# Optimization experiments

Measured on AMD Instinct MI355X. Metric: run time of the kernel, lower is better.

The kernel has to match this reference:

```python
import jax, jax.numpy as jnp
import numpy as np

B, T, D, H, W = 128, 1024, 32, 64, 128
C = D + 1            # control_size = data_size + 1
O = H * C            # cvf MLP output size


def _linear_params(k, out_f, in_f):
    lim = 1.0 / np.sqrt(in_f)
    kw, kb = jax.random.split(k)
    Wm = jax.random.uniform(kw, (out_f, in_f), minval=-lim, maxval=lim, dtype=jnp.float32)
    b = jax.random.uniform(kb, (out_f,), minval=-lim, maxval=lim, dtype=jnp.float32)
    return Wm, b


def setup_inputs() -> dict:
    key = jax.random.key(0)
    ks = jax.random.split(key, 8)
    # initial MLP: (D+1) -> W -> W -> H, relu hidden
    iW0, ib0 = _linear_params(ks[0], W, D + 1)
    iW1, ib1 = _linear_params(ks[1], W, W)
    iW2, ib2 = _linear_params(ks[2], H, W)
    # cvf MLP: (H+1) -> W -> W -> H*C, lipswish hidden, tanh final
    vW0, vb0 = _linear_params(ks[3], W, H + 1)
    vW1, vb1 = _linear_params(ks[4], W, W)
    vW2, vb2 = _linear_params(ks[5], O, W)
    # readout: H -> 1
    rW, rb = _linear_params(ks[6], 1, H)
    ts = jnp.arange(T, dtype=jnp.float32)
    ys = jax.random.normal(ks[7], (B, T, D), dtype=jnp.float32)
    return dict(ts=ts, ys=ys,
                iW0=iW0, ib0=ib0, iW1=iW1, ib1=ib1, iW2=iW2, ib2=ib2,
                vW0=vW0, vb0=vb0, vW1=vb1 * 0 + vW1, vb1=vb1, vW2=vW2, vb2=vb2,
                rW=rW, rb=rb)


def _lipswish(x):
    return 0.909 * jax.nn.silu(x)


def reference(ts, ys, iW0, ib0, iW1, ib1, iW2, ib2,
              vW0, vb0, vW1, vb1, vW2, vb2, rW, rb):
    b, t_len, d = ys.shape
    h = iW2.shape[0]
    c = d + 1

    def initial_mlp(x):  # [B, D+1] -> [B, H]
        z = jax.nn.relu(x @ iW0.T + ib0)
        z = jax.nn.relu(z @ iW1.T + ib1)
        return z @ iW2.T + ib2

    def vf(t, y):  # scalar t, y [B,H] -> [B,H,C]
        inp = jnp.concatenate([jnp.full((y.shape[0], 1), t, y.dtype), y], axis=1)
        z = _lipswish(inp @ vW0.T + vb0)
        z = _lipswish(z @ vW1.T + vb1)
        out = jnp.tanh(z @ vW2.T + vb2)
        return out.reshape(y.shape[0], h, c)

    # control path values x(t_i) = [t_i, y_i]; no NaNs so interpolation fixups are no-ops
    xs = jnp.concatenate([jnp.broadcast_to(ts[None, :, None], (b, t_len, 1)), ys], axis=2)  # [B,T,C]
    y0 = initial_mlp(xs[:, 0])
    vf0 = vf(ts[0], y0)

    # constant step dt=1 aligned with grid -> control increments are consecutive diffs
    dxs = jnp.swapaxes(xs[:, 1:] - xs[:, :-1], 0, 1)  # [T-1,B,C]
    t1s = ts[1:]

    def step(carry, inp):
        y, yhat, v = carry
        t1, dx = inp
        # ReversibleHeun: yhat1 = 2*y - yhat + f(t0,yhat0)·dx ; y1 = y + 0.5*(f0+f1)·dx
        yhat1 = 2.0 * y - yhat + jnp.einsum('bhc,bc->bh', v, dx)
        v1 = vf(t1, yhat1)
        y1 = y + 0.5 * jnp.einsum('bhc,bc->bh', v + v1, dx)
        return (y1, yhat1, v1), None

    (yT, _, _), _ = jax.lax.scan(step, (y0, y0, vf0), (t1s, dxs))
    return yT @ rW.T + rb  # [B,1]
```

## Files before the change

kernel.cpp:

```cpp
#include <hip/hip_runtime.h>
#include <math.h>

constexpr int kB  = 128;
constexpr int kT  = 1024;
constexpr int kD  = 32;
constexpr int kH  = 64;
constexpr int kW  = 128;
constexpr int kC  = kD + 1;
constexpr int kO  = kH * kC;
constexpr int kIN = kH + 1;
constexpr int BLOCK = 1024;

constexpr int WS_W2  = 0;
constexpr int WS_W1  = 135168;
constexpr int WS_W0  = 143360;
constexpr int WS_SC2 = 147584;
constexpr int WS_SC1 = 149696;
constexpr int WS_SC0 = 149824;
constexpr int WS_TOT = 149952;

__device__ __forceinline__ float fast_sigmoid(float x) { return 1.0f / (1.0f + __expf(-x)); }
__device__ __forceinline__ float lipswish_f(float x)   { return 0.909f * x * fast_sigmoid(x); }
__device__ __forceinline__ float fast_tanh(float x) {
    float ax = fabsf(x);
    float e  = __expf(2.0f * ax);
    float r  = 1.0f - 2.0f / (e + 1.0f);
    return copysignf(r, x);
}
__device__ __forceinline__ float dot4(float4 a, float4 b) {
    return a.x * b.x + a.y * b.y + a.z * b.z + a.w * b.w;
}
__device__ __forceinline__ float fma2i(unsigned u, float z0, float z1, float acc) {
    int lo = (int)(short)(u & 0xffffu);
    int hi = ((int)u) >> 16;
    acc += (float)lo * z0 + (float)hi * z1;
    return acc;
}
__device__ __forceinline__ float fma8i(uint4 u, float4 zl, float4 zh, float acc) {
    acc = fma2i(u.x, zl.x, zl.y, acc);
    acc = fma2i(u.y, zl.z, zl.w, acc);
    acc = fma2i(u.z, zh.x, zh.y, acc);
    acc = fma2i(u.w, zh.z, zh.w, acc);
    return acc;
}
__device__ __forceinline__ int q15(float w, float inv) {
    float q = rintf(w * inv);
    q = fmaxf(-32767.0f, fminf(32767.0f, q));
    return (int)q;
}
__device__ __forceinline__ unsigned pack16(int a, int b) {
    return ((unsigned)a & 0xffffu) | ((unsigned)b << 16);
}

__global__ __launch_bounds__(64)
void prep_kernel(const float* __restrict__ vW0, const float* __restrict__ vW1,
                 const float* __restrict__ vW2, unsigned* __restrict__ ws)
{
    const int row  = blockIdx.x;
    const int lane = threadIdx.x;
    float* scf = (float*)ws;

    if (row < kO) {
        const float* src = vW2 + (size_t)row * kW;
        float m = fmaxf(fabsf(src[lane]), fabsf(src[lane + 64]));
        #pragma unroll
        for (int s = 1; s < 64; s <<= 1) m = fmaxf(m, __shfl_xor(m, s));
        float inv = (m > 0.0f) ? 32767.0f / m : 0.0f;
        if (lane == 0) scf[WS_SC2 + row] = (m > 0.0f) ? m / 32767.0f : 0.0f;
        int w = lane;
        unsigned pk = pack16(q15(src[2 * w], inv), q15(src[2 * w + 1], inv));
        int R = row >> 6, r = row & 63, q = w >> 2, e = w & 3;
        ws[WS_W2 + (((R * 16 + q) * 64 + r) << 2) + e] = pk;
    } else if (row < kO + kW) {
        int r = row - kO;
        const float* src = vW1 + (size_t)r * kW;
        float m = fmaxf(fabsf(src[lane]), fabsf(src[lane + 64]));
        #pragma unroll
        for (int s = 1; s < 64; s <<= 1) m = fmaxf(m, __shfl_xor(m, s));
        float inv = (m > 0.0f) ? 32767.0f / m : 0.0f;
        if (lane == 0) scf[WS_SC1 + r] = (m > 0.0f) ? m / 32767.0f : 0.0f;
        int w = lane;
        ws[WS_W1 + r * 64 + w] = pack16(q15(src[2 * w], inv), q15(src[2 * w + 1], inv));
    } else {
        int r = row - kO - kW;
        const float* src = vW0 + (size_t)r * kIN;
        float m = fabsf(src[lane]);
        if (lane == 0) m = fmaxf(m, fabsf(src[64]));
        #pragma unroll
        for (int s = 1; s < 64; s <<= 1) m = fmaxf(m, __shfl_xor(m, s));
        float inv = (m > 0.0f) ? 32767.0f / m : 0.0f;
        if (lane == 0) scf[WS_SC0 + r] = (m > 0.0f) ? m / 32767.0f : 0.0f;
        if (lane < 33) {
            int c0 = 2 * lane, c1 = 2 * lane + 1;
            int qa = q15(src[c0], inv);
            int qb = (c1 < kIN) ? q15(src[c1], inv) : 0;
            ws[WS_W0 + r * 33 + lane] = pack16(qa, qb);
        }
    }
}

template <int QI>
__global__ __launch_bounds__(BLOCK)
void cde_kernel(
    const float* __restrict__ ts,  const float* __restrict__ ys,
    const float* __restrict__ iW0, const float* __restrict__ ib0,
    const float* __restrict__ iW1, const float* __restrict__ ib1,
    const float* __restrict__ iW2, const float* __restrict__ ib2,
    const float* __restrict__ vW0, const float* __restrict__ vb0,
    const float* __restrict__ vW1, const float* __restrict__ vb1,
    const float* __restrict__ vW2, const float* __restrict__ vb2,
    const float* __restrict__ rW,  const float* __restrict__ rb,
    const unsigned* __restrict__ wsb,
    float* __restrict__ out)
{
    const int b  = blockIdx.x;
    const int t  = threadIdx.x;
    const int r8 = t >> 3;
    const int g  = t & 7;
    const int wv = t >> 6;
    const int ln = t & 63;

    __shared__ __align__(16) float s_v[kO];
    __shared__ __align__(16) float s_z1[kW], s_z2[kW];
    __shared__ __align__(16) float s_inp[kIN + 1];
    __shared__ float s_y[kH], s_yhat[kH], s_e[kH];
    __shared__ float s_dx[kC];

    const float*    ysb   = ys + (size_t)b * kT * kD;
    const uint4*    wsW2q = (const uint4*)(wsb + WS_W2);
    const unsigned* wsW1  = wsb + WS_W1;
    const unsigned* wsW0  = wsb + WS_W0;
    const float*    scf   = (const float*)wsb;

    const float bA  = vb2[t];
    const float bB  = vb2[t + 1024];
    const float bTl = (t < 512) ? vb2[2048 + r8] : 0.0f;
    const float b0r = vb0[r8];
    const float b1r = vb1[r8];
    const float sA  = QI ? scf[WS_SC2 + t] : 0.0f;
    const float sB  = QI ? scf[WS_SC2 + t + 1024] : 0.0f;
    const float sTl = (QI && t < 512) ? scf[WS_SC2 + 2048 + r8] : 0.0f;
    const float s0r = QI ? scf[WS_SC0 + r8] : 0.0f;
    const float s1r = QI ? scf[WS_SC1 + r8] : 0.0f;

    float x_reg = 0.0f, x_next = 0.0f;
    if (t < kC) {
        x_reg  = (t == 0) ? ts[0] : ysb[t - 1];
        x_next = (t == 0) ? ts[1] : ysb[kD + (t - 1)];
        s_dx[t] = x_reg;
    }
    if (t == 0) s_inp[kIN] = 0.0f;
    __syncthreads();

    if (t < kW) {
        const float* wrow = iW0 + t * kC;
        float acc = ib0[t];
        #pragma unroll
        for (int c = 0; c < kC; c++) acc += wrow[c] * s_dx[c];
        s_z1[t] = fmaxf(acc, 0.0f);
    }
    __syncthreads();
    if (t < kW) {
        const float4* wr = (const float4*)(iW1 + t * kW);
        const float4* z4 = (const float4*)s_z1;
        float acc = ib1[t];
        #pragma unroll 8
        for (int q = 0; q < kW / 4; q++) acc += dot4(wr[q], z4[q]);
        s_z2[t] = fmaxf(acc, 0.0f);
    }
    __syncthreads();
    if (t < kH) {
        const float4* wr = (const float4*)(iW2 + t * kW);
        const float4* z4 = (const float4*)s_z2;
        float acc = ib2[t];
        #pragma unroll 8
        for (int q = 0; q < kW / 4; q++) acc += dot4(wr[q], z4[q]);
        s_y[t] = acc; s_yhat[t] = acc;
        s_inp[1 + t] = acc;
    }
    if (t == 0) s_inp[0] = x_reg;
    __syncthreads();

    for (int i = 0; i < kT; i++) {
        {
            float acc = 0.0f;
            if (QI) {
                const unsigned* rowp = wsW0 + r8 * 33;
                #pragma unroll
                for (int m = 0; m < 5; m++) {
                    int p = g + 8 * m;
                    if (p < 33) acc = fma2i(rowp[p], s_inp[2 * p], s_inp[2 * p + 1], acc);
                }
            } else {
                const float* rowp = vW0 + r8 * kIN;
                #pragma unroll
                for (int m = 0; m < 5; m++) {
                    int p = g + 8 * m;
                    if (p < 33) {
                        float w0 = rowp[2 * p];
                        float w1 = (2 * p + 1 < kIN) ? rowp[2 * p + 1] : 0.0f;
                        acc += w0 * s_inp[2 * p] + w1 * s_inp[2 * p + 1];
                    }
                }
            }
            acc += __shfl_xor(acc, 1);
            acc += __shfl_xor(acc, 2);
            acc += __shfl_xor(acc, 4);
            if (g == 0) s_z1[r8] = lipswish_f(b0r + (QI ? s0r * acc : acc));
        }
        __syncthreads();
        {
            float acc = 0.0f;
            #pragma unroll
            for (int m = 0; m < 2; m++) {
                int ch = g + 8 * m;
                int c0 = 8 * ch;
                const float4* z4 = (const float4*)(s_z1 + c0);
                float4 za = z4[0], zb = z4[1];
                if (QI) {
                    uint4 u = *(const uint4*)(wsW1 + r8 * 64 + 4 * ch);
                    acc = fma8i(u, za, zb, acc);
                } else {
                    const float* wr = vW1 + r8 * kW + c0;
                    acc += dot4(*(const float4*)wr, za) + dot4(*(const float4*)(wr + 4), zb);
                }
            }
            acc += __shfl_xor(acc, 1);
            acc += __shfl_xor(acc, 2);
            acc += __shfl_xor(acc, 4);
            if (g == 0) s_z2[r8] = lipswish_f(b1r + (QI ? s1r * acc : acc));
        }
        __syncthreads();
        {
            float acc0 = 0.0f, acc1 = 0.0f;
            if (QI) {
                const uint4* pA = wsW2q + (size_t)(wv * 16) * 64 + ln;
                const uint4* pB = wsW2q + (size_t)((wv + 16) * 16) * 64 + ln;
                #pragma unroll 2
                for (int m = 0; m < 8; m++) {
                    const float4* z4 = (const float4*)(s_z2 + 16 * m);
                    float4 z0 = z4[0], z1 = z4[1], z2 = z4[2], z3 = z4[3];
                    uint4 a0 = pA[(2 * m) * 64],     a1 = pA[(2 * m + 1) * 64];
                    uint4 c0 = pB[(2 * m) * 64],     c1 = pB[(2 * m + 1) * 64];
                    acc0 = fma8i(a0, z0, z1, acc0);
                    acc0 = fma8i(a1, z2, z3, acc0);
                    acc1 = fma8i(c0, z0, z1, acc1);
                    acc1 = fma8i(c1, z2, z3, acc1);
                }
                s_v[t]        = fast_tanh(bA + sA * acc0);
                s_v[t + 1024] = fast_tanh(bB + sB * acc1);
            } else {
                #pragma unroll 2
                for (int m = 0; m < 8; m++) {
                    const float4* z4 = (const float4*)(s_z2 + 16 * m);
                    float4 z0 = z4[0], z1 = z4[1], z2 = z4[2], z3 = z4[3];
                    const float4* rA = (const float4*)(vW2 + (size_t)t * kW + 16 * m);
                    const float4* rB = (const float4*)(vW2 + (size_t)(t + 1024) * kW + 16 * m);
                    acc0 += dot4(rA[0], z0) + dot4(rA[1], z1) + dot4(rA[2], z2) + dot4(rA[3], z3);
                    acc1 += dot4(rB[0], z0) + dot4(rB[1], z1) + dot4(rB[2], z2) + dot4(rB[3], z3);
                }
                s_v[t]        = fast_tanh(bA + acc0);
                s_v[t + 1024] = fast_tanh(bB + acc1);
            }
        }
        if (t < 512) {
            int c0 = 16 * g;
            const float4* z4 = (const float4*)(s_z2 + c0);
            float4 z0 = z4[0], z1 = z4[1], z2 = z4[2], z3 = z4[3];
            float acc = 0.0f;
            if (QI) {
                uint4 u0 = wsW2q[(size_t)(32 * 16 + 2 * g) * 64 + r8];
                uint4 u1 = wsW2q[(size_t)(32 * 16 + 2 * g + 1) * 64 + r8];
                acc = fma8i(u0, z0, z1, acc);
                acc = fma8i(u1, z2, z3, acc);
            } else {
                const float4* wr = (const float4*)(vW2 + (size_t)(2048 + r8) * kW + c0);
                acc += dot4(wr[0], z0) + dot4(wr[1], z1) + dot4(wr[2], z2) + dot4(wr[3], z3);
            }
            acc += __shfl_xor(acc, 1);
            acc += __shfl_xor(acc, 2);
            acc += __shfl_xor(acc, 4);
            if (g == 0) s_v[2048 + r8] = fast_tanh(bTl + (QI ? sTl * acc : acc));
        }
        __syncthreads();

        if (i > 0 && t < kH) {
            const float* vr = s_v + t * kC;
            float acc = 0.0f;
            #pragma unroll
            for (int c = 0; c < kC; c++) acc += vr[c] * s_dx[c];
            s_y[t] += 0.5f * (s_e[t] + acc);
        }
        __syncthreads();

        if (i < kT - 1) {
            if (t < kC) {
                float xi = x_next;
                s_dx[t] = xi - x_reg;
                x_reg = xi;
                if (i + 2 < kT)
                    x_next = (t == 0) ? ts[i + 2] : ysb[(size_t)(i + 2) * kD + (t - 1)];
            }
            __syncthreads();
            if (t < kH) {
                const float* vr = s_v + t * kC;
                float e = 0.0f;
                #pragma unroll
                for (int c = 0; c < kC; c++) e += vr[c] * s_dx[c];
                s_e[t] = e;
                float yh = 2.0f * s_y[t] - s_yhat[t] + e;
                s_yhat[t] = yh;
                s_inp[1 + t] = yh;
            }
            if (t == 0) s_inp[0] = x_reg;
            __syncthreads();
        }
    }

    __syncthreads();
    if (t == 0) {
        float acc = rb[0];
        #pragma unroll
        for (int h = 0; h < kH; h++) acc += s_y[h] * rW[h];
        out[b] = acc;
    }
}

extern "C" void kernel_launch(void* const* d_in, const int* in_sizes, int n_in,
                              void* d_out, int out_size, void* d_ws, size_t ws_size,
                              hipStream_t stream)
{
    const float* ts  = (const float*)d_in[0];
    const float* ys  = (const float*)d_in[1];
    const float* iW0 = (const float*)d_in[2];
    const float* ib0 = (const float*)d_in[3];
    const float* iW1 = (const float*)d_in[4];
    const float* ib1 = (const float*)d_in[5];
    const float* iW2 = (const float*)d_in[6];
    const float* ib2 = (const float*)d_in[7];
    const float* vW0 = (const float*)d_in[8];
    const float* vb0 = (const float*)d_in[9];
    const float* vW1 = (const float*)d_in[10];
    const float* vb1 = (const float*)d_in[11];
    const float* vW2 = (const float*)d_in[12];
    const float* vb2 = (const float*)d_in[13];
    const float* rW  = (const float*)d_in[14];
    const float* rb  = (const float*)d_in[15];
    float* out = (float*)d_out;
    unsigned* ws = (unsigned*)d_ws;

    if (ws_size >= (size_t)WS_TOT * 4) {
        hipLaunchKernelGGL(prep_kernel, dim3(kO + kW + kW), dim3(64), 0, stream,
                           vW0, vW1, vW2, ws);
        hipLaunchKernelGGL((cde_kernel<1>), dim3(kB), dim3(BLOCK), 0, stream,
                           ts, ys, iW0, ib0, iW1, ib1, iW2, ib2,
                           vW0, vb0, vW1, vb1, vW2, vb2, rW, rb, ws, out);
    } else {
        hipLaunchKernelGGL((cde_kernel<0>), dim3(kB), dim3(BLOCK), 0, stream,
                           ts, ys, iW0, ib0, iW1, ib1, iW2, ib2,
                           vW0, vb0, vW1, vb1, vW2, vb2, rW, rb, ws, out);
    }
}
```

Before: 6.456 ms.

## Split each batch's vector field across two cooperating blocks with flag sync

Adds a kernel that launches two blocks per batch element. Each block computes half of the cvf output rows (1056 of 2112) and updates half of the hidden state. The halves of yhat are exchanged every step through global memory, using agent-scope release/acquire flags and a double-buffered exchange buffer. This aims to halve the per-step final-layer work per block and use all 256 CUs instead of 128, at the cost of a cross-block spin-wait each timestep. Correctness depends on both blocks of a pair being co-resident.

```diff
diff --git a/kernel.cpp b/kernel.cpp
--- a/kernel.cpp
+++ b/kernel.cpp
@@ -18,6 +18,9 @@
 constexpr int WS_SC1 = 149696;
 constexpr int WS_SC0 = 149824;
 constexpr int WS_TOT = 149952;
+constexpr int WS_XB   = 149952;
+constexpr int WS_FLAG = 166336;
+constexpr int WS_TOT2 = 166592;
 
 __device__ __forceinline__ float fast_sigmoid(float x) { return 1.0f / (1.0f + __expf(-x)); }
 __device__ __forceinline__ float lipswish_f(float x)   { return 0.909f * x * fast_sigmoid(x); }
@@ -61,6 +64,7 @@
     float* scf = (float*)ws;
 
     if (row < kO) {
+        if (row < 4) ws[WS_FLAG + row * 64 + lane] = 0;
         const float* src = vW2 + (size_t)row * kW;
         float m = fmaxf(fabsf(src[lane]), fabsf(src[lane + 64]));
         #pragma unroll
@@ -99,9 +103,240 @@
     }
 }
 
+__global__ __launch_bounds__(BLOCK)
+void cde_split(
+    const float* __restrict__ ts,  const float* __restrict__ ys,
+    const float* __restrict__ iW0, const float* __restrict__ ib0,
+    const float* __restrict__ iW1, const float* __restrict__ ib1,
+    const float* __restrict__ iW2, const float* __restrict__ ib2,
+    const float* __restrict__ vW0, const float* __restrict__ vb0,
+    const float* __restrict__ vW1, const float* __restrict__ vb1,
+    const float* __restrict__ vW2, const float* __restrict__ vb2,
+    const float* __restrict__ rW,  const float* __restrict__ rb,
+    unsigned* wsm,
+    float* __restrict__ out)
+{
+    const int batch = blockIdx.x & 127;
+    const int R     = blockIdx.x >> 7;
+    const int t  = threadIdx.x;
+    const int r8 = t >> 3;
+    const int g  = t & 7;
+
+    __shared__ __align__(16) float s_v[1056];
+    __shared__ __align__(16) float s_z1[kW], s_z2[kW];
+    __shared__ __align__(16) float s_inp[kIN + 1];
+    __shared__ float s_y[32], s_yhat[32], s_e[32];
+    __shared__ float s_x[3][34];
+
+    const float*    ysb   = ys + (size_t)batch * kT * kD;
+    const unsigned* wsb   = wsm;
+    const uint4*    wsW2q = (const uint4*)(wsb + WS_W2);
+    const unsigned* wsW1  = wsb + WS_W1;
+    const unsigned* wsW0  = wsb + WS_W0;
+    const float*    scf   = (const float*)wsb;
+    float*    xbf = (float*)(wsm + WS_XB) + (size_t)batch * 128;
+    unsigned* flg = wsm + WS_FLAG + batch * 2;
+
+    const int rowM = R * 1056 + t;
+    const float bM = vb2[rowM];
+    const float sM = scf[WS_SC2 + rowM];
+    const int rowT = R * 1056 + 1024 + (t >> 3);
+    const float bT = (t < 256) ? vb2[rowT] : 0.0f;
+    const float sT = (t < 256) ? scf[WS_SC2 + rowT] : 0.0f;
+    const float b0r = vb0[r8];
+    const float b1r = vb1[r8];
+    const float s0r = scf[WS_SC0 + r8];
+    const float s1r = scf[WS_SC1 + r8];
+
+    float x_next = 0.0f;
+    const float* yptr = nullptr;
+    if (t < kC) {
+        float x0v, x1v;
+        if (t == 0) { x0v = ts[0]; x1v = ts[1]; }
+        else {
+            const float* p = ysb + (t - 1);
+            x0v = p[0]; x1v = p[kD]; yptr = p + 2 * kD;
+        }
+        s_x[0][t] = x0v; s_x[1][t] = x1v; s_x[2][t] = 0.0f;
+        x_next = x1v;
+    }
+    if (t == 0) s_inp[kIN] = 0.0f;
+    __syncthreads();
+
+    if (t < kW) {
+        const float* wrow = iW0 + t * kC;
+        float acc = ib0[t];
+        #pragma unroll
+        for (int c = 0; c < kC; c++) acc += wrow[c] * s_x[0][c];
+        s_z1[t] = fmaxf(acc, 0.0f);
+    }
+    __syncthreads();
+    if (t < kW) {
+        const float4* wr = (const float4*)(iW1 + t * kW);
+        const float4* z4 = (const float4*)s_z1;
+        float acc = ib1[t];
+        #pragma unroll 8
+        for (int q = 0; q < kW / 4; q++) acc += dot4(wr[q], z4[q]);
+        s_z2[t] = fmaxf(acc, 0.0f);
+    }
+    __syncthreads();
+    if (t < kH) {
+        const float4* wr = (const float4*)(iW2 + t * kW);
+        const float4* z4 = (const float4*)s_z2;
+        float acc = ib2[t];
+        #pragma unroll 8
+        for (int q = 0; q < kW / 4; q++) acc += dot4(wr[q], z4[q]);
+        s_inp[1 + t] = acc;
+        if ((t >> 5) == R) {
+            s_y[t & 31] = acc; s_yhat[t & 31] = acc;
+        }
+    }
+    if (t == 0) s_inp[0] = ts[0];
+    __syncthreads();
+
+    const uint4* pW = wsW2q + ((size_t)(rowM >> 6) * 16) * 64 + (rowM & 63);
+
+    for (int i = 0; i < kT; i++) {
+        const int i0  = i % 3;
+        const int ip1 = (i + 1) % 3;
+        const int im1 = (i + 2) % 3;
+
+        {
+            float acc = 0.0f;
+            const unsigned* rowp = wsW0 + r8 * 33;
+            #pragma unroll
+            for (int m = 0; m < 5; m++) {
+                int p = g + 8 * m;
+                if (p < 33) acc = fma2i(rowp[p], s_inp[2 * p], s_inp[2 * p + 1], acc);
+            }
+            acc += __shfl_xor(acc, 1);
+            acc += __shfl_xor(acc, 2);
+            acc += __shfl_xor(acc, 4);
+            if (g == 0) s_z1[r8] = lipswish_f(b0r + s0r * acc);
+        }
+        if (t < kC && i + 1 < kT) {
+            s_x[ip1][t] = x_next;
+            if (i + 2 < kT) {
+                if (t == 0) x_next = ts[i + 2];
+                else { x_next = *yptr; yptr += kD; }
+            }
+        }
+        __syncthreads();
+
+        {
+            float acc = 0.0f;
+            #pragma unroll
+            for (int m = 0; m < 2; m++) {
+                int ch = g + 8 * m;
+                const float4* z4 = (const float4*)(s_z1 + 8 * ch);
+                float4 za = z4[0], zb = z4[1];
+                uint4 u = *(const uint4*)(wsW1 + r8 * 64 + 4 * ch);
+                acc = fma8i(u, za, zb, acc);
+            }
+            acc += __shfl_xor(acc, 1);
+            acc += __shfl_xor(acc, 2);
+            acc += __shfl_xor(acc, 4);
+            if (g == 0) s_z2[r8] = lipswish_f(b1r + s1r * acc);
+        }
+        __syncthreads();
+
+        {
+            float acc = 0.0f;
+            #pragma unroll 2
+            for (int m = 0; m < 8; m++) {
+                uint4 w0 = pW[(2 * m) * 64], w1 = pW[(2 * m + 1) * 64];
+                const float4* z4 = (const float4*)(s_z2 + 16 * m);
+                acc = fma8i(w0, z4[0], z4[1], acc);
+                acc = fma8i(w1, z4[2], z4[3], acc);
+            }
+            s_v[t] = fast_tanh(bM + sM * acc);
+        }
+        if (t < 256) {
+            const float4* z4 = (const float4*)(s_z2 + 16 * g);
+            float4 z0 = z4[0], z1 = z4[1], z2 = z4[2], z3 = z4[3];
+            const size_t qb = ((size_t)(rowT >> 6) * 16) * 64 + (rowT & 63);
+            uint4 u0 = wsW2q[qb + (size_t)(2 * g) * 64];
+            uint4 u1 = wsW2q[qb + (size_t)(2 * g + 1) * 64];
+            float acc = fma8i(u0, z0, z1, 0.0f);
+            acc = fma8i(u1, z2, z3, acc);
+            acc += __shfl_xor(acc, 1);
+            acc += __shfl_xor(acc, 2);
+            acc += __shfl_xor(acc, 4);
+            if (g == 0) s_v[1024 + (t >> 3)] = fast_tanh(bT + sT * acc);
+        }
+        __syncthreads();
+
+        if (t < 32) {
+            const float* vr = s_v + t * kC;
+            const float* xm = s_x[im1];
+            const float* xc = s_x[i0];
+            const float* xp = s_x[ip1];
+            float dA = 0.0f, dB = 0.0f;
+            #pragma unroll
+            for (int c = 0; c < kC; c++) {
+                float vv = vr[c];
+                dA += vv * (xc[c] - xm[c]);
+                dB += vv * (xp[c] - xc[c]);
+            }
+            if (i > 0) s_y[t] += 0.5f * (s_e[t] + dA);
+            if (i < kT - 1) {
+                s_e[t] = dB;
+                float yh = 2.0f * s_y[t] - s_yhat[t] + dB;
+                s_yhat[t] = yh;
+                const int hg = R * 32 + t;
+                s_inp[1 + hg] = yh;
+                __hip_atomic_store(&xbf[(i & 1) * 64 + hg], yh,
+                                   __ATOMIC_RELAXED, __HIP_MEMORY_SCOPE_AGENT);
+            }
+        }
+        if (i < kT - 1) {
+            if (t == 0) {
+                s_inp[0] = s_x[ip1][0];
+                asm volatile("s_waitcnt vmcnt(0)" ::: "memory");
+                __hip_atomic_store(flg + R, (unsigned)(i + 1),
+                                   __ATOMIC_RELEASE, __HIP_MEMORY_SCOPE_AGENT);
+            }
+            if (t < 32) {
+                const unsigned tgt = (unsigned)(i + 1);
+                while (__hip_atomic_load(flg + (1 - R), __ATOMIC_ACQUIRE,
+                                         __HIP_MEMORY_SCOPE_AGENT) < tgt)
+                    __builtin_amdgcn_s_sleep(2);
+                const int ph = (1 - R) * 32 + t;
+                float pv = __hip_atomic_load(&xbf[(i & 1) * 64 + ph],
+                                             __ATOMIC_RELAXED, __HIP_MEMORY_SCOPE_AGENT);
+                s_inp[1 + ph] = pv;
+            }
+        }
+        __syncthreads();
+    }
+
+    if (R == 1) {
+        if (t == 0) {
+            float ph = 0.0f;
+            #pragma unroll
+            for (int h = 0; h < 32; h++) ph += s_y[h] * rW[32 + h];
+            __hip_atomic_store(&xbf[127], ph, __ATOMIC_RELAXED, __HIP_MEMORY_SCOPE_AGENT);
+            asm volatile("s_waitcnt vmcnt(0)" ::: "memory");
+            __hip_atomic_store(flg + 1, 1024u, __ATOMIC_RELEASE, __HIP_MEMORY_SCOPE_AGENT);
+        }
+    } else {
+        if (t == 0) {
+            float pl = rb[0];
+            #pragma unroll
+            for (int h = 0; h < 32; h++) pl += s_y[h] * rW[h];
+            while (__hip_atomic_load(flg + 1, __ATOMIC_ACQUIRE,
+                                     __HIP_MEMORY_SCOPE_AGENT) < 1024u)
+                __builtin_amdgcn_s_sleep(2);
+            float ph = __hip_atomic_load(&xbf[127], __ATOMIC_RELAXED,
+                                         __HIP_MEMORY_SCOPE_AGENT);
+            out[batch] = pl + ph;
+        }
+    }
+}
+
 template <int QI>
 __global__ __launch_bounds__(BLOCK)
-void cde_kernel(
+void cde_mono(
     const float* __restrict__ ts,  const float* __restrict__ ys,
     const float* __restrict__ iW0, const float* __restrict__ ib0,
     const float* __restrict__ iW1, const float* __restrict__ ib1,
@@ -349,14 +584,20 @@
     float* out = (float*)d_out;
     unsigned* ws = (unsigned*)d_ws;
 
-    if (ws_size >= (size_t)WS_TOT * 4) {
+    if (ws_size >= (size_t)WS_TOT2 * 4) {
         hipLaunchKernelGGL(prep_kernel, dim3(kO + kW + kW), dim3(64), 0, stream,
                            vW0, vW1, vW2, ws);
-        hipLaunchKernelGGL((cde_kernel<1>), dim3(kB), dim3(BLOCK), 0, stream,
+        hipLaunchKernelGGL(cde_split, dim3(2 * kB), dim3(BLOCK), 0, stream,
+                           ts, ys, iW0, ib0, iW1, ib1, iW2, ib2,
+                           vW0, vb0, vW1, vb1, vW2, vb2, rW, rb, ws, out);
+    } else if (ws_size >= (size_t)WS_TOT * 4) {
+        hipLaunchKernelGGL(prep_kernel, dim3(kO + kW + kW), dim3(64), 0, stream,
+                           vW0, vW1, vW2, ws);
+        hipLaunchKernelGGL((cde_mono<1>), dim3(kB), dim3(BLOCK), 0, stream,
                            ts, ys, iW0, ib0, iW1, ib1, iW2, ib2,
                            vW0, vb0, vW1, vb1, vW2, vb2, rW, rb, ws, out);
     } else {
-        hipLaunchKernelGGL((cde_kernel<0>), dim3(kB), dim3(BLOCK), 0, stream,
+        hipLaunchKernelGGL((cde_mono<0>), dim3(kB), dim3(BLOCK), 0, stream,
                            ts, ys, iW0, ib0, iW1, ib1, iW2, ib2,
                            vW0, vb0, vW1, vb1, vW2, vb2, rW, rb, ws, out);
     }
```

Measured after the change: 10.38 ms. 60.8% more time.
